# Performance work log

Measured on AMD Instinct MI355X. Metric: run time of the kernel, lower is better.

The kernel has to match this reference:

```python
import jax, jax.numpy as jnp
import numpy as np

NUM_KEYPOINTS = 2048
SAMPLE_RADIUS = 1.6
NUM_SECTORS = 6
NEG = jnp.float32(-1e10)
POS = jnp.float32(1e10)


def setup_inputs() -> dict:
    key = jax.random.key(0)
    kxy, kz, kc, kcz, kd, ky = jax.random.split(key, 6)
    B, N, M = 2, 65536, 128
    pts_xy = jax.random.uniform(kxy, (B, N, 2), minval=-70.0, maxval=70.0)
    pts_z = jax.random.uniform(kz, (B, N, 1), minval=-3.0, maxval=1.0)
    points = jnp.concatenate([pts_xy, pts_z], axis=-1)  # [B,N,3]
    ctr_xy = jax.random.uniform(kc, (B, M, 2), minval=-60.0, maxval=60.0)
    ctr_z = jax.random.uniform(kcz, (B, M, 1), minval=-2.0, maxval=0.0)
    dims = jax.random.uniform(kd, (B, M, 3), minval=1.0, maxval=4.5)
    yaw = jax.random.uniform(ky, (B, M, 1), minval=-np.pi, maxval=np.pi)
    rois = jnp.concatenate([ctr_xy, ctr_z, dims, yaw], axis=-1)  # [B,M,7]
    return {"points": points, "rois": rois}


def _masked_fps(xyz, mask, K):
    """Farthest point sampling restricted to mask; returns K indices into xyz.
    Matches mmcv furthest_point_sample: squared distances, start at first point."""
    first = jnp.argmax(mask)  # first valid point in original order
    dmin = jnp.where(mask, POS, NEG)

    def step(carry, _):
        dmin, last = carry
        d = jnp.sum((xyz - xyz[last]) ** 2, axis=-1)
        dmin = jnp.minimum(dmin, jnp.where(mask, d, NEG))
        nxt = jnp.argmax(dmin)
        return (dmin, nxt), nxt

    (_, _), rest = jax.lax.scan(step, (dmin, first), None, length=K - 1)
    return jnp.concatenate([first[None], rest])  # [K]


def _spc_single(points, rois):
    """points: [N,3] float, rois: [M,7]. Returns [NUM_KEYPOINTS,3]."""
    N = points.shape[0]
    K = NUM_KEYPOINTS
    # geometric center: z += dz/2 (done in forward before sampling)
    rois = rois.at[:, 2].add(rois[:, 5] * 0.5)
    # --- sample_points_with_roi: point-to-ROI-center distance filter ---
    diff = points[:, None, :] - rois[None, :, 0:3]          # [N,M,3]
    dist = jnp.linalg.norm(diff, axis=-1)                   # [N,M]
    min_dis = jnp.min(dist, axis=-1)
    min_idx = jnp.argmin(dist, axis=-1)
    roi_max_dim = jnp.linalg.norm(rois[min_idx, 3:6] * 0.5, axis=-1)
    valid = min_dis < roi_max_dim + SAMPLE_RADIUS           # [N]
    total = jnp.maximum(jnp.sum(valid), 1)
    # --- sector_fps ---
    sector_size = 2.0 * np.pi / NUM_SECTORS
    angles = jnp.arctan2(points[:, 1], points[:, 0]) + np.pi
    sector = jnp.clip(jnp.floor(angles / sector_size), 0, NUM_SECTORS).astype(jnp.int32)
    masks = valid[None, :] & (sector[None, :] == jnp.arange(NUM_SECTORS)[:, None])  # [S,N]
    cnt = jnp.sum(masks, axis=-1)                           # [S]
    # per-sector budget: min(cnt_k, ceil(cnt_k / total * K)), 0 for empty sectors
    n_k = jnp.minimum(cnt, jnp.ceil(cnt.astype(jnp.float32) * K / total).astype(cnt.dtype))
    fps_idx = jax.vmap(_masked_fps, in_axes=(None, 0, None))(points, masks, K)  # [S,K]
    # concatenate the first n_k picks of each sector in sector order
    offsets = jnp.concatenate([jnp.zeros((1,), n_k.dtype), jnp.cumsum(n_k)[:-1]])
    pos = offsets[:, None] + jnp.arange(K)[None, :]          # [S,K] slot in concat order
    keep = jnp.arange(K)[None, :] < n_k[:, None]
    pos = jnp.where(keep, pos, K)                            # out-of-range -> dropped
    buf = jnp.zeros((K,), jnp.int32)
    buf = buf.at[pos.reshape(-1)].set(fps_idx.reshape(-1).astype(jnp.int32), mode='drop')
    # truncate / cyclic-repeat to exactly K keypoints
    s_total = jnp.maximum(jnp.sum(n_k), 1)
    out_idx = buf[jnp.arange(K) % s_total]
    return points[out_idx]                                   # [K,3]


def reference(points, rois):
    return jax.vmap(_spc_single)(points, rois)  # [B,K,3]
```

## Files before the change

kernel.cpp:

```cpp
#include <hip/hip_runtime.h>
#include <cmath>
#include <cstdint>

#pragma clang fp contract(off)

#define B_ 2
#define N_ 65536
#define M_ 128
#define K_ 2048
#define S_ 6
#define NBLK 256
#define CT 256
#define FPS_T 256
#define NW 4
#define RMAX 16
#define CAP (FPS_T * RMAX)

#define PI_F 3.14159265358979323846f
#define SS_F 1.0471975511965976f

__device__ __forceinline__ unsigned long long wave_max_u64_dpp(unsigned long long key) {
#define DPP_STEP(CTRL)                                                          \
    {                                                                           \
        unsigned lo = (unsigned)key, hi = (unsigned)(key >> 32);                \
        unsigned olo = (unsigned)__builtin_amdgcn_update_dpp(0, (int)lo, CTRL, 0xf, 0xf, true); \
        unsigned ohi = (unsigned)__builtin_amdgcn_update_dpp(0, (int)hi, CTRL, 0xf, 0xf, true); \
        unsigned long long o = ((unsigned long long)ohi << 32) | olo;           \
        if (o > key) key = o;                                                   \
    }
    DPP_STEP(0x111)
    DPP_STEP(0x112)
    DPP_STEP(0x114)
    DPP_STEP(0x118)
    DPP_STEP(0x142)
    DPP_STEP(0x143)
#undef DPP_STEP
    return key;
}

__global__ __launch_bounds__(CT)
void k_classify(const float* __restrict__ points, const float* __restrict__ rois,
                int* __restrict__ sec_id, int* __restrict__ blkcnt) {
    __shared__ float4 sroi[M_];
    __shared__ int lc[8];
    int blk = blockIdx.x;
    int gid = blk * CT + threadIdx.x;
    int b = gid >> 16;
    if (threadIdx.x < M_) {
        const float* r = rois + ((size_t)b * M_ + threadIdx.x) * 7;
        float cz = r[2] + r[5] * 0.5f;
        float hx = r[3] * 0.5f, hy = r[4] * 0.5f, hz = r[5] * 0.5f;
        sroi[threadIdx.x] = make_float4(r[0], r[1], cz, sqrtf((hx*hx + hy*hy) + hz*hz));
    }
    if (threadIdx.x < 8) lc[threadIdx.x] = 0;
    __syncthreads();

    const float* p = points + (size_t)gid * 3;
    float px = p[0], py = p[1], pz = p[2];
    float best = 1e30f; int bi = 0;
    for (int m = 0; m < M_; m++) {
        float4 c = sroi[m];
        float dx = px - c.x, dy = py - c.y, dz = pz - c.z;
        float d = sqrtf((dx*dx + dy*dy) + dz*dz);
        if (d < best) { best = d; bi = m; }
    }
    bool valid = best < (sroi[bi].w + 1.6f);

    float a = atan2f(py, px) + PI_F;
    float fs = floorf(a / SS_F);
    fs = fminf(fmaxf(fs, 0.0f), 6.0f);
    int sec = (int)fs;

    sec_id[gid] = valid ? sec : -1;
    if (valid) atomicAdd(&lc[sec], 1);
    __syncthreads();
    if (threadIdx.x < 8) blkcnt[blk * 8 + threadIdx.x] = lc[threadIdx.x];
}

__global__ void k_plan(const int* __restrict__ blkcnt, int* __restrict__ bbase,
                       int* __restrict__ cnt, int* __restrict__ offv,
                       int* __restrict__ n_needed, int* __restrict__ sec_base,
                       int* __restrict__ s_total) {
    __shared__ int scnt[2][8];
    int t = threadIdx.x;
    if (t < 16) scnt[t >> 3][t & 7] = 0;
    __syncthreads();
    if (t < 14) {
        int b = t / 7, s = t % 7;
        int run = 0;
        for (int j = 0; j < NBLK; j++) {
            int blk = b * NBLK + j;
            int c = blkcnt[blk * 8 + s];
            if (s < 6) bbase[blk * 6 + s] = run;
            run += c;
        }
        scnt[b][s] = run;
        cnt[b * 8 + s] = run;
    }
    __syncthreads();
    if (t < B_) {
        int b = t;
        int total = 0;
        for (int s = 0; s < 7; s++) total += scnt[b][s];
        if (total < 1) total = 1;
        int sb = 0, snk = 0;
        for (int s = 0; s < 6; s++) {
            int cs = scnt[b][s];
            int nk = (int)ceilf((float)cs * 2048.0f / (float)total);
            if (nk > cs) nk = cs;
            offv[b * 6 + s] = snk;
            int need = 0;
            if (snk < K_) { need = K_ - snk; if (need > nk) need = nk; }
            n_needed[b * 6 + s] = need;
            sec_base[b * 6 + s] = sb;
            sb += cs; snk += nk;
        }
        s_total[b] = (snk < 1) ? 1 : snk;
    }
}

__global__ __launch_bounds__(CT)
void k_compact(const float* __restrict__ points, const int* __restrict__ sec_id,
               const int* __restrict__ sec_base, const int* __restrict__ bbase,
               int* __restrict__ comp_idx, float4* __restrict__ comp_xyz) {
    __shared__ int lc[4 * 6];
    __shared__ int sbase[6], blkb[6];
    int blk = blockIdx.x;
    int b = blk >> 8;
    int tid = threadIdx.x, lane = tid & 63, wid = tid >> 6;
    if (tid < 6) sbase[tid] = sec_base[b * 6 + tid];
    else if (tid >= 64 && tid < 70) blkb[tid - 64] = bbase[blk * 6 + (tid - 64)];
    int gid = blk * CT + tid;
    int sec = sec_id[gid];
    unsigned long long mymask = 0;
    for (int s = 0; s < 6; s++) {
        unsigned long long m = __ballot(sec == s);
        if (sec == s) mymask = m;
        if (lane == 0) lc[wid * 6 + s] = __popcll(m);
    }
    __syncthreads();
    if (sec >= 0 && sec < 6) {
        int woff = 0;
        for (int w = 0; w < wid; w++) woff += lc[w * 6 + sec];
        int rank = __popcll(mymask & ((1ull << lane) - 1ull));
        int addr = b * N_ + sbase[sec] + blkb[sec] + woff + rank;
        const float* p = points + (size_t)gid * 3;
        comp_idx[addr] = gid & (N_ - 1);
        comp_xyz[addr] = make_float4(p[0], p[1], p[2], 0.0f);
    }
}

__global__ __launch_bounds__(FPS_T, 1)
void k_fps(const int* __restrict__ cnt, const int* __restrict__ sec_base,
           const int* __restrict__ offv, const int* __restrict__ n_needed,
           const float4* __restrict__ comp_xyz,
           float* __restrict__ dmin_g, int* __restrict__ buf) {
    __shared__ float4 sxyz[CAP];
    __shared__ unsigned long long skey[2][NW];
    int b = blockIdx.x / S_, s = blockIdx.x % S_;
    int need = n_needed[b * 6 + s];
    if (need <= 0) return;
    int cs = cnt[b * 8 + s];
    int base = b * N_ + sec_base[b * 6 + s];
    const float4* cxyz = comp_xyz + base;
    int off = b * K_ + offv[b * 6 + s];
    int tid = threadIdx.x, lane = tid & 63, wid = tid >> 6;

    if (tid == 0) buf[off] = base;
    if (cs <= CAP) {
        float px[RMAX], py[RMAX], pz[RMAX], dmv[RMAX];
        #pragma unroll
        for (int r = 0; r < RMAX; r++) {
            if (r * FPS_T < cs) {
                int i = tid + r * FPS_T;
                if (i < cs) {
                    float4 q = cxyz[i];
                    sxyz[i] = q;
                    px[r] = q.x; py[r] = q.y; pz[r] = q.z;
                    dmv[r] = 1e10f;
                }
            }
        }
        __syncthreads();
        if (need == 1) return;
        float4 l4 = sxyz[0];
        float lx = l4.x, ly = l4.y, lz = l4.z;

        #pragma unroll 1
        for (int k = 1; k < need; k++) {
            unsigned long long key = 0;
            #pragma unroll
            for (int r = 0; r < RMAX; r++) {
                if (r * FPS_T < cs) {
                    int i = tid + r * FPS_T;
                    if (i < cs) {
                        float dx = px[r] - lx, dy = py[r] - ly, dz = pz[r] - lz;
                        float d = (dx*dx + dy*dy) + dz*dz;
                        float nd = fminf(dmv[r], d);
                        dmv[r] = nd;
                        unsigned long long kk =
                            ((unsigned long long)__float_as_uint(nd) << 32) | (unsigned)(~(unsigned)i);
                        if (kk > key) key = kk;
                    }
                }
            }
            key = wave_max_u64_dpp(key);
            int par = k & 1;
            if (lane == 63) skey[par][wid] = key;
            __syncthreads();
            unsigned long long bk = skey[par][0];
            if (skey[par][1] > bk) bk = skey[par][1];
            if (skey[par][2] > bk) bk = skey[par][2];
            if (skey[par][3] > bk) bk = skey[par][3];
            int bix = (int)(~(unsigned)(bk & 0xFFFFFFFFull));
            if (tid == 0) buf[off + k] = base + bix;
            float4 n4 = sxyz[bix];
            lx = n4.x; ly = n4.y; lz = n4.z;
        }
    } else {
        float* dm = dmin_g + base;
        __syncthreads();
        if (need == 1) return;
        float4 f0 = cxyz[0];
        float lx = f0.x, ly = f0.y, lz = f0.z;
        #pragma unroll 1
        for (int k = 1; k < need; k++) {
            unsigned long long key = 0;
            for (int i = tid; i < cs; i += FPS_T) {
                float4 q = cxyz[i];
                float dx = q.x - lx, dy = q.y - ly, dz = q.z - lz;
                float d = (dx*dx + dy*dy) + dz*dz;
                float prev = (k == 1) ? 1e10f : dm[i];
                float nd = fminf(prev, d);
                dm[i] = nd;
                unsigned long long kk =
                    ((unsigned long long)__float_as_uint(nd) << 32) | (unsigned)(~(unsigned)i);
                if (kk > key) key = kk;
            }
            key = wave_max_u64_dpp(key);
            int par = k & 1;
            if (lane == 63) skey[par][wid] = key;
            __syncthreads();
            unsigned long long bk = skey[par][0];
            if (skey[par][1] > bk) bk = skey[par][1];
            if (skey[par][2] > bk) bk = skey[par][2];
            if (skey[par][3] > bk) bk = skey[par][3];
            int bix = (int)(~(unsigned)(bk & 0xFFFFFFFFull));
            if (tid == 0) buf[off + k] = base + bix;
            float4 n4 = cxyz[bix];
            lx = n4.x; ly = n4.y; lz = n4.z;
        }
    }
}

__global__ void k_out(const float* __restrict__ points, const int* __restrict__ buf,
                      const int* __restrict__ comp_idx, const int* __restrict__ s_total,
                      float* __restrict__ out) {
    int i = blockIdx.x * 256 + threadIdx.x;
    if (i >= B_ * K_) return;
    int b = i / K_, j = i % K_;
    int st = s_total[b];
    int g = buf[b * K_ + (j % st)];
    int idx = comp_idx[g];
    const float* p = points + ((size_t)b * N_ + idx) * 3;
    float* o = out + (size_t)i * 3;
    o[0] = p[0]; o[1] = p[1]; o[2] = p[2];
}

extern "C" void kernel_launch(void* const* d_in, const int* in_sizes, int n_in,
                              void* d_out, int out_size, void* d_ws, size_t ws_size,
                              hipStream_t stream) {
    const float* points = (const float*)d_in[0];
    const float* rois   = (const float*)d_in[1];
    float* out = (float*)d_out;

    char* w = (char*)d_ws;
    auto carve = [&](size_t bytes) -> char* {
        char* p = w; w += (bytes + 255) & ~(size_t)255; return p;
    };
    int*    sec_id   = (int*)   carve((size_t)B_ * N_ * sizeof(int));
    int*    blkcnt   = (int*)   carve((size_t)B_ * NBLK * 8 * sizeof(int));
    int*    bbase    = (int*)   carve((size_t)B_ * NBLK * 6 * sizeof(int));
    int*    cnt      = (int*)   carve((size_t)B_ * 8 * sizeof(int));
    int*    offv     = (int*)   carve((size_t)B_ * 6 * sizeof(int));
    int*    n_needed = (int*)   carve((size_t)B_ * 6 * sizeof(int));
    int*    sec_base = (int*)   carve((size_t)B_ * 6 * sizeof(int));
    int*    s_total  = (int*)   carve((size_t)B_ * sizeof(int));
    int*    buf      = (int*)   carve((size_t)B_ * K_ * sizeof(int));
    int*    comp_idx = (int*)   carve((size_t)B_ * N_ * sizeof(int));
    float4* comp_xyz = (float4*)carve((size_t)B_ * N_ * sizeof(float4));
    float*  dmin_g   = (float*) carve((size_t)B_ * N_ * sizeof(float));

    hipLaunchKernelGGL(k_classify, dim3(B_ * NBLK), dim3(CT), 0, stream,
                       points, rois, sec_id, blkcnt);
    hipLaunchKernelGGL(k_plan, dim3(1), dim3(64), 0, stream,
                       blkcnt, bbase, cnt, offv, n_needed, sec_base, s_total);
    hipLaunchKernelGGL(k_compact, dim3(B_ * NBLK), dim3(CT), 0, stream,
                       points, sec_id, sec_base, bbase, comp_idx, comp_xyz);
    hipLaunchKernelGGL(k_fps, dim3(B_ * S_), dim3(FPS_T), 0, stream,
                       cnt, sec_base, offv, n_needed, comp_xyz, dmin_g, buf);
    hipLaunchKernelGGL(k_out, dim3((B_ * K_ + 255) / 256), dim3(256), 0, stream,
                       points, buf, comp_idx, s_total, out);
}
```

Measured before the change: 492.3 us.

## Carry winner coordinates through FPS reductions and size register tiles per sector

The FPS argmax reduction now carries the winning point's xyz alongside its key through DPP and the cross-wave exchange. This removes the dependent shared-memory lookup of the next centre on each serial iteration. Register tiles are templated on the sector's point count, so small sectors do less unrolled work. Picks are buffered in LDS and written to the output directly from the FPS kernel, leaving a fill kernel to handle only the cyclic-repeat tail. In exchange, each DPP step moves three extra floats and the kernel has more code paths.

Measured after the change: 583.7 us. 1.19x slower.

```diff
diff --git a/kernel.cpp b/kernel.cpp
--- a/kernel.cpp
+++ b/kernel.cpp
@@ -13,11 +13,39 @@
 #define CT 256
 #define FPS_T 256
 #define NW 4
-#define RMAX 16
-#define CAP (FPS_T * RMAX)
+#define CAP (FPS_T * 16)
 
 #define PI_F 3.14159265358979323846f
 #define SS_F 1.0471975511965976f
+
+struct Pick { unsigned long long key; float x, y, z; };
+
+struct FpsShared {
+    alignas(16) unsigned long long rk[2][NW];
+    alignas(16) float rx[2][NW];
+    alignas(16) float ry[2][NW];
+    alignas(16) float rz[2][NW];
+    int    pick[K_];
+    float4 pxyz[K_];
+};
+
+__device__ __forceinline__ Pick wave_pick_max(Pick p) {
+#define STEP(CTRL)                                                              \
+    {                                                                           \
+        unsigned lo = (unsigned)p.key, hi = (unsigned)(p.key >> 32);            \
+        unsigned olo = (unsigned)__builtin_amdgcn_update_dpp(0, (int)lo, CTRL, 0xf, 0xf, true); \
+        unsigned ohi = (unsigned)__builtin_amdgcn_update_dpp(0, (int)hi, CTRL, 0xf, 0xf, true); \
+        int ox = __builtin_amdgcn_update_dpp(0, __float_as_int(p.x), CTRL, 0xf, 0xf, true); \
+        int oy = __builtin_amdgcn_update_dpp(0, __float_as_int(p.y), CTRL, 0xf, 0xf, true); \
+        int oz = __builtin_amdgcn_update_dpp(0, __float_as_int(p.z), CTRL, 0xf, 0xf, true); \
+        unsigned long long ok = ((unsigned long long)ohi << 32) | olo;          \
+        if (ok > p.key) { p.key = ok; p.x = __int_as_float(ox);                 \
+                          p.y = __int_as_float(oy); p.z = __int_as_float(oz); } \
+    }
+    STEP(0x111) STEP(0x112) STEP(0x114) STEP(0x118) STEP(0x142) STEP(0x143)
+#undef STEP
+    return p;
+}
 
 __device__ __forceinline__ unsigned long long wave_max_u64_dpp(unsigned long long key) {
 #define DPP_STEP(CTRL)                                                          \
@@ -28,12 +56,8 @@
         unsigned long long o = ((unsigned long long)ohi << 32) | olo;           \
         if (o > key) key = o;                                                   \
     }
-    DPP_STEP(0x111)
-    DPP_STEP(0x112)
-    DPP_STEP(0x114)
-    DPP_STEP(0x118)
-    DPP_STEP(0x142)
-    DPP_STEP(0x143)
+    DPP_STEP(0x111) DPP_STEP(0x112) DPP_STEP(0x114)
+    DPP_STEP(0x118) DPP_STEP(0x142) DPP_STEP(0x143)
 #undef DPP_STEP
     return key;
 }
@@ -80,7 +104,7 @@
 __global__ void k_plan(const int* __restrict__ blkcnt, int* __restrict__ bbase,
                        int* __restrict__ cnt, int* __restrict__ offv,
                        int* __restrict__ n_needed, int* __restrict__ sec_base,
-                       int* __restrict__ s_total) {
+                       int* __restrict__ s_total2) {
     __shared__ int scnt[2][8];
     int t = threadIdx.x;
     if (t < 16) scnt[t >> 3][t & 7] = 0;
@@ -115,7 +139,8 @@
             sec_base[b * 6 + s] = sb;
             sb += cs; snk += nk;
         }
-        s_total[b] = (snk < 1) ? 1 : snk;
+        s_total2[b * 2]     = (snk < 1) ? 1 : snk;
+        s_total2[b * 2 + 1] = snk;
     }
 }
 
@@ -150,13 +175,84 @@
     }
 }
 
-__global__ __launch_bounds__(FPS_T, 1)
+template<int R>
+__device__ __forceinline__
+void fps_fast(FpsShared& sh, const float4* __restrict__ cxyz, int cs, int need,
+              int base, int off, int* __restrict__ buf, float* __restrict__ out,
+              int tid, int lane, int wid) {
+    float px[R], py[R], pz[R], dmv[R];
+    #pragma unroll
+    for (int r = 0; r < R; r++) {
+        int i = tid + r * FPS_T;
+        if (i < cs) {
+            float4 q = cxyz[i];
+            px[r] = q.x; py[r] = q.y; pz[r] = q.z;
+            dmv[r] = 1e10f;
+        }
+    }
+    float4 f0 = cxyz[0];
+    if (tid == 0) { sh.pick[0] = 0; sh.pxyz[0] = f0; }
+    float lx = f0.x, ly = f0.y, lz = f0.z;
+
+    #pragma unroll 1
+    for (int k = 1; k < need; k++) {
+        float bv = -1.0f, bx = 0.0f, by = 0.0f, bz = 0.0f; int bi = 0;
+        #pragma unroll
+        for (int r = 0; r < R; r++) {
+            int i = tid + r * FPS_T;
+            if (i < cs) {
+                float dx = px[r] - lx, dy = py[r] - ly, dz = pz[r] - lz;
+                float d = (dx*dx + dy*dy) + dz*dz;
+                float nd = fminf(dmv[r], d);
+                dmv[r] = nd;
+                if (nd > bv) { bv = nd; bi = i; bx = px[r]; by = py[r]; bz = pz[r]; }
+            }
+        }
+        Pick p;
+        p.key = (bv >= 0.0f)
+              ? (((unsigned long long)__float_as_uint(bv) << 32) | (unsigned)(~(unsigned)bi))
+              : 0ull;
+        p.x = bx; p.y = by; p.z = bz;
+        p = wave_pick_max(p);
+        int par = k & 1;
+        if (lane == 63) {
+            sh.rk[par][wid] = p.key;
+            sh.rx[par][wid] = p.x; sh.ry[par][wid] = p.y; sh.rz[par][wid] = p.z;
+        }
+        __syncthreads();
+        ulonglong2 k01 = *(const ulonglong2*)&sh.rk[par][0];
+        ulonglong2 k23 = *(const ulonglong2*)&sh.rk[par][2];
+        float4 xv = *(const float4*)&sh.rx[par][0];
+        float4 yv = *(const float4*)&sh.ry[par][0];
+        float4 zv = *(const float4*)&sh.rz[par][0];
+        unsigned long long bk = k01.x; float wx = xv.x, wy = yv.x, wz = zv.x;
+        if (k01.y > bk) { bk = k01.y; wx = xv.y; wy = yv.y; wz = zv.y; }
+        if (k23.x > bk) { bk = k23.x; wx = xv.z; wy = yv.z; wz = zv.z; }
+        if (k23.y > bk) { bk = k23.y; wx = xv.w; wy = yv.w; wz = zv.w; }
+        if (tid == 0) {
+            int bix = (int)(~(unsigned)(bk & 0xFFFFFFFFull));
+            sh.pick[k] = bix;
+            sh.pxyz[k] = make_float4(wx, wy, wz, 0.0f);
+        }
+        lx = wx; ly = wy; lz = wz;
+    }
+    __syncthreads();
+    #pragma unroll 1
+    for (int i = tid; i < need; i += FPS_T) {
+        buf[off + i] = base + sh.pick[i];
+        float4 q = sh.pxyz[i];
+        float* o = out + (size_t)(off + i) * 3;
+        o[0] = q.x; o[1] = q.y; o[2] = q.z;
+    }
+}
+
+__global__ __launch_bounds__(FPS_T, 3)
 void k_fps(const int* __restrict__ cnt, const int* __restrict__ sec_base,
            const int* __restrict__ offv, const int* __restrict__ n_needed,
            const float4* __restrict__ comp_xyz,
-           float* __restrict__ dmin_g, int* __restrict__ buf) {
-    __shared__ float4 sxyz[CAP];
-    __shared__ unsigned long long skey[2][NW];
+           float* __restrict__ dmin_g, int* __restrict__ buf,
+           float* __restrict__ out) {
+    __shared__ FpsShared sh;
     int b = blockIdx.x / S_, s = blockIdx.x % S_;
     int need = n_needed[b * 6 + s];
     if (need <= 0) return;
@@ -166,66 +262,21 @@
     int off = b * K_ + offv[b * 6 + s];
     int tid = threadIdx.x, lane = tid & 63, wid = tid >> 6;
 
-    if (tid == 0) buf[off] = base;
-    if (cs <= CAP) {
-        float px[RMAX], py[RMAX], pz[RMAX], dmv[RMAX];
-        #pragma unroll
-        for (int r = 0; r < RMAX; r++) {
-            if (r * FPS_T < cs) {
-                int i = tid + r * FPS_T;
-                if (i < cs) {
-                    float4 q = cxyz[i];
-                    sxyz[i] = q;
-                    px[r] = q.x; py[r] = q.y; pz[r] = q.z;
-                    dmv[r] = 1e10f;
-                }
-            }
-        }
-        __syncthreads();
-        if (need == 1) return;
-        float4 l4 = sxyz[0];
-        float lx = l4.x, ly = l4.y, lz = l4.z;
-
-        #pragma unroll 1
-        for (int k = 1; k < need; k++) {
-            unsigned long long key = 0;
-            #pragma unroll
-            for (int r = 0; r < RMAX; r++) {
-                if (r * FPS_T < cs) {
-                    int i = tid + r * FPS_T;
-                    if (i < cs) {
-                        float dx = px[r] - lx, dy = py[r] - ly, dz = pz[r] - lz;
-                        float d = (dx*dx + dy*dy) + dz*dz;
-                        float nd = fminf(dmv[r], d);
-                        dmv[r] = nd;
-                        unsigned long long kk =
-                            ((unsigned long long)__float_as_uint(nd) << 32) | (unsigned)(~(unsigned)i);
-                        if (kk > key) key = kk;
-                    }
-                }
-            }
-            key = wave_max_u64_dpp(key);
-            int par = k & 1;
-            if (lane == 63) skey[par][wid] = key;
-            __syncthreads();
-            unsigned long long bk = skey[par][0];
-            if (skey[par][1] > bk) bk = skey[par][1];
-            if (skey[par][2] > bk) bk = skey[par][2];
-            if (skey[par][3] > bk) bk = skey[par][3];
-            int bix = (int)(~(unsigned)(bk & 0xFFFFFFFFull));
-            if (tid == 0) buf[off + k] = base + bix;
-            float4 n4 = sxyz[bix];
-            lx = n4.x; ly = n4.y; lz = n4.z;
-        }
-    } else {
+    if      (cs <=  2 * FPS_T) fps_fast< 2>(sh, cxyz, cs, need, base, off, buf, out, tid, lane, wid);
+    else if (cs <=  4 * FPS_T) fps_fast< 4>(sh, cxyz, cs, need, base, off, buf, out, tid, lane, wid);
+    else if (cs <=  6 * FPS_T) fps_fast< 6>(sh, cxyz, cs, need, base, off, buf, out, tid, lane, wid);
+    else if (cs <=  8 * FPS_T) fps_fast< 8>(sh, cxyz, cs, need, base, off, buf, out, tid, lane, wid);
+    else if (cs <= 12 * FPS_T) fps_fast<12>(sh, cxyz, cs, need, base, off, buf, out, tid, lane, wid);
+    else if (cs <= 16 * FPS_T) fps_fast<16>(sh, cxyz, cs, need, base, off, buf, out, tid, lane, wid);
+    else {
         float* dm = dmin_g + base;
-        __syncthreads();
-        if (need == 1) return;
         float4 f0 = cxyz[0];
+        if (tid == 0) { sh.pick[0] = 0; sh.pxyz[0] = f0; }
         float lx = f0.x, ly = f0.y, lz = f0.z;
         #pragma unroll 1
         for (int k = 1; k < need; k++) {
             unsigned long long key = 0;
+            #pragma unroll 1
             for (int i = tid; i < cs; i += FPS_T) {
                 float4 q = cxyz[i];
                 float dx = q.x - lx, dy = q.y - ly, dz = q.z - lz;
@@ -239,31 +290,46 @@
             }
             key = wave_max_u64_dpp(key);
             int par = k & 1;
-            if (lane == 63) skey[par][wid] = key;
+            if (lane == 63) sh.rk[par][wid] = key;
             __syncthreads();
-            unsigned long long bk = skey[par][0];
-            if (skey[par][1] > bk) bk = skey[par][1];
-            if (skey[par][2] > bk) bk = skey[par][2];
-            if (skey[par][3] > bk) bk = skey[par][3];
+            unsigned long long bk = sh.rk[par][0];
+            if (sh.rk[par][1] > bk) bk = sh.rk[par][1];
+            if (sh.rk[par][2] > bk) bk = sh.rk[par][2];
+            if (sh.rk[par][3] > bk) bk = sh.rk[par][3];
             int bix = (int)(~(unsigned)(bk & 0xFFFFFFFFull));
-            if (tid == 0) buf[off + k] = base + bix;
             float4 n4 = cxyz[bix];
+            if (tid == 0) { sh.pick[k] = bix; sh.pxyz[k] = n4; }
             lx = n4.x; ly = n4.y; lz = n4.z;
         }
-    }
-}
-
-__global__ void k_out(const float* __restrict__ points, const int* __restrict__ buf,
-                      const int* __restrict__ comp_idx, const int* __restrict__ s_total,
-                      float* __restrict__ out) {
+        __syncthreads();
+        #pragma unroll 1
+        for (int i = tid; i < need; i += FPS_T) {
+            buf[off + i] = base + sh.pick[i];
+            float4 q = sh.pxyz[i];
+            float* o = out + (size_t)(off + i) * 3;
+            o[0] = q.x; o[1] = q.y; o[2] = q.z;
+        }
+    }
+}
+
+__global__ void k_fill(const float* __restrict__ points, const int* __restrict__ buf,
+                       const int* __restrict__ comp_idx, const int* __restrict__ s_total2,
+                       float* __restrict__ out) {
     int i = blockIdx.x * 256 + threadIdx.x;
     if (i >= B_ * K_) return;
     int b = i / K_, j = i % K_;
-    int st = s_total[b];
+    int st = s_total2[b * 2];
+    int snk = s_total2[b * 2 + 1];
+    if (j < st && snk > 0) return;
+    float* o = out + (size_t)i * 3;
+    if (snk <= 0) {
+        const float* p = points + (size_t)b * N_ * 3;
+        o[0] = p[0]; o[1] = p[1]; o[2] = p[2];
+        return;
+    }
     int g = buf[b * K_ + (j % st)];
     int idx = comp_idx[g];
     const float* p = points + ((size_t)b * N_ + idx) * 3;
-    float* o = out + (size_t)i * 3;
     o[0] = p[0]; o[1] = p[1]; o[2] = p[2];
 }
 
@@ -285,7 +351,7 @@
     int*    offv     = (int*)   carve((size_t)B_ * 6 * sizeof(int));
     int*    n_needed = (int*)   carve((size_t)B_ * 6 * sizeof(int));
     int*    sec_base = (int*)   carve((size_t)B_ * 6 * sizeof(int));
-    int*    s_total  = (int*)   carve((size_t)B_ * sizeof(int));
+    int*    s_total2 = (int*)   carve((size_t)B_ * 2 * sizeof(int));
     int*    buf      = (int*)   carve((size_t)B_ * K_ * sizeof(int));
     int*    comp_idx = (int*)   carve((size_t)B_ * N_ * sizeof(int));
     float4* comp_xyz = (float4*)carve((size_t)B_ * N_ * sizeof(float4));
@@ -294,11 +360,11 @@
     hipLaunchKernelGGL(k_classify, dim3(B_ * NBLK), dim3(CT), 0, stream,
                        points, rois, sec_id, blkcnt);
     hipLaunchKernelGGL(k_plan, dim3(1), dim3(64), 0, stream,
-                       blkcnt, bbase, cnt, offv, n_needed, sec_base, s_total);
+                       blkcnt, bbase, cnt, offv, n_needed, sec_base, s_total2);
     hipLaunchKernelGGL(k_compact, dim3(B_ * NBLK), dim3(CT), 0, stream,
                        points, sec_id, sec_base, bbase, comp_idx, comp_xyz);
     hipLaunchKernelGGL(k_fps, dim3(B_ * S_), dim3(FPS_T), 0, stream,
-                       cnt, sec_base, offv, n_needed, comp_xyz, dmin_g, buf);
-    hipLaunchKernelGGL(k_out, dim3((B_ * K_ + 255) / 256), dim3(256), 0, stream,
-                       points, buf, comp_idx, s_total, out);
-}
+                       cnt, sec_base, offv, n_needed, comp_xyz, dmin_g, buf, out);
+    hipLaunchKernelGGL(k_fill, dim3((B_ * K_ + 255) / 256), dim3(256), 0, stream,
+                       points, buf, comp_idx, s_total2, out);
+}
```
